# Optimization experiments

Hardware: AMD Instinct MI355X
Metric: run time of the kernel (lower is better)

Reference implementation:

```python
import jax, jax.numpy as jnp
import numpy as np

B, T, C = 512, 128, 384   # batch, seq (== block_size), embed_dim
H, D = 6, 64              # n_heads, head_size
BLOCK_SIZE = 128


def setup_inputs() -> dict:
    key = jax.random.key(0)
    ks = jax.random.split(key, 6)
    s = C ** -0.5  # init scale, values irrelevant to correctness
    x = jax.random.normal(ks[0], (B, T, C), dtype=jnp.float32)
    Wq = jax.random.normal(ks[1], (H, C, D), dtype=jnp.float32) * s
    Wk = jax.random.normal(ks[2], (H, C, D), dtype=jnp.float32) * s
    Wv = jax.random.normal(ks[3], (H, C, D), dtype=jnp.float32) * s
    Wp = jax.random.normal(ks[4], (H * D, C), dtype=jnp.float32) * s
    bp = jax.random.normal(ks[5], (C,), dtype=jnp.float32) * 0.01
    return {"x": x, "Wq": Wq, "Wk": Wk, "Wv": Wv, "Wp": Wp, "bp": bp}


def reference(x, Wq, Wk, Wv, Wp, bp):
    # Forward of MultiHeadAttentionClass (eval mode: dropout disabled).
    # Heads are vectorized instead of the original Python per-head loop.
    Bx, Tx, Cx = x.shape
    x = x[:, :BLOCK_SIZE, :]                       # truncate to block_size
    t = x.shape[1]
    q = jnp.einsum('btc,hcd->bhtd', x, Wq)         # [B,H,T,D]
    k = jnp.einsum('btc,hcd->bhtd', x, Wk)
    v = jnp.einsum('btc,hcd->bhtd', x, Wv)
    scores = jnp.einsum('bhtd,bhsd->bhts', q, k) * (D ** -0.5)  # [B,H,T,T]
    causal = jnp.tril(jnp.ones((t, t), dtype=bool))
    scores = jnp.where(causal[None, None], scores, -jnp.inf)
    wei = jax.nn.softmax(scores, axis=-1)
    out = jnp.einsum('bhts,bhsd->bhtd', wei, v)    # [B,H,T,D]
    out = out.transpose(0, 2, 1, 3).reshape(x.shape[0], t, H * D)  # concat heads
    out = out @ Wp + bp                            # projection to embed_dim
    return out
```

## Files before the change

### kernel.cpp

```cpp
#include <hip/hip_runtime.h>

#define NB 512
#define NTOK 128
#define NC 384
#define NH 6
#define ND 64

typedef short s16x8 __attribute__((ext_vector_type(8)));
typedef float f32x4 __attribute__((ext_vector_type(4)));

#define MFMA16(a, b, c) __builtin_amdgcn_mfma_f32_16x16x32_bf16((a), (b), (c), 0, 0, 0)

static __device__ __forceinline__ unsigned short f2bf(float f) {
  unsigned int u = __builtin_bit_cast(unsigned int, f);
  u = (u + 0x7FFFu + ((u >> 16) & 1u)) >> 16;
  return (unsigned short)u;
}

__global__ __launch_bounds__(256) void convert_weights(
    const float* __restrict__ Wq, const float* __restrict__ Wk,
    const float* __restrict__ Wv, const float* __restrict__ Wp,
    unsigned short* __restrict__ wqkvT, unsigned short* __restrict__ wpT) {
  int idx = blockIdx.x * 256 + threadIdx.x;
  const int NQKV = 3 * NH * ND * NC;
  if (idx < NQKV) {
    int c = idx % NC;
    int d = (idx / NC) % ND;
    int h = (idx / (NC * ND)) % NH;
    int m = idx / (NC * ND * NH);
    const float* W = (m == 0) ? Wq : (m == 1) ? Wk : Wv;
    wqkvT[idx] = f2bf(W[(h * NC + c) * ND + d]);
  } else {
    int j = idx - NQKV;
    int cc = j / NC, r = j % NC;
    wpT[j] = f2bf(Wp[r * NC + cc]);
  }
}

struct SP1 { unsigned short xs[128][40]; unsigned short w[3][64][40]; };
struct SP3 { unsigned short p[128][72]; };

__global__ __launch_bounds__(256, 2) void attn_fused(
    const float* __restrict__ x, const unsigned short* __restrict__ wqkvT,
    unsigned short* __restrict__ O) {
  const int h = blockIdx.x >> 9;
  const int b = blockIdx.x & 511;
  const int tid = threadIdx.x;
  const int lane = tid & 63;
  const int l15 = lane & 15;
  const int lg = lane >> 4;
  const int r0 = (tid >> 6) * 32;

  __shared__ __align__(16) union { SP1 p1; SP3 p3; } su;
  __shared__ __align__(16) unsigned short qs[128][72];
  __shared__ __align__(16) unsigned short ks[128][72];
  __shared__ __align__(16) unsigned short vts[64][144];

  f32x4 accq[2][4], acck[2][4], accv[2][4];
#pragma unroll
  for (int i = 0; i < 2; ++i)
#pragma unroll
    for (int j = 0; j < 4; ++j) {
      accq[i][j] = f32x4{0.f, 0.f, 0.f, 0.f};
      acck[i][j] = f32x4{0.f, 0.f, 0.f, 0.f};
      accv[i][j] = f32x4{0.f, 0.f, 0.f, 0.f};
    }

  const float* xb = x + (size_t)b * (NTOK * NC);
  const unsigned short* wb = wqkvT + h * (ND * NC);

  const int xr = tid >> 3;
  const int xc = (tid & 7) * 4;
  const int wn = tid >> 2;
  const int wc = (tid & 3) * 8;

  for (int kc = 0; kc < 12; ++kc) {
    const int c0 = kc * 32;
    __syncthreads();
#pragma unroll
    for (int s = 0; s < 4; ++s) {
      int row = xr + 32 * s;
      float4 f = *(const float4*)(xb + row * NC + c0 + xc);
      union { unsigned short h4[4]; uint2 u; } t;
      t.h4[0] = f2bf(f.x); t.h4[1] = f2bf(f.y); t.h4[2] = f2bf(f.z); t.h4[3] = f2bf(f.w);
      *(uint2*)&su.p1.xs[row][xc] = t.u;
    }
#pragma unroll
    for (int m = 0; m < 3; ++m) {
      s16x8 w8 = *(const s16x8*)(wb + m * (NH * ND * NC) + wn * NC + c0 + wc);
      *(s16x8*)&su.p1.w[m][wn][wc] = w8;
    }
    __syncthreads();
    s16x8 a0 = *(const s16x8*)&su.p1.xs[r0 + l15][lg * 8];
    s16x8 a1 = *(const s16x8*)&su.p1.xs[r0 + 16 + l15][lg * 8];
#pragma unroll
    for (int nt = 0; nt < 4; ++nt) {
      s16x8 bq = *(const s16x8*)&su.p1.w[0][nt * 16 + l15][lg * 8];
      accq[0][nt] = MFMA16(a0, bq, accq[0][nt]);
      accq[1][nt] = MFMA16(a1, bq, accq[1][nt]);
      s16x8 bk = *(const s16x8*)&su.p1.w[1][nt * 16 + l15][lg * 8];
      acck[0][nt] = MFMA16(a0, bk, acck[0][nt]);
      acck[1][nt] = MFMA16(a1, bk, acck[1][nt]);
      s16x8 bv = *(const s16x8*)&su.p1.w[2][nt * 16 + l15][lg * 8];
      accv[0][nt] = MFMA16(a0, bv, accv[0][nt]);
      accv[1][nt] = MFMA16(a1, bv, accv[1][nt]);
    }
  }

#pragma unroll
  for (int mt = 0; mt < 2; ++mt)
#pragma unroll
    for (int nt = 0; nt < 4; ++nt) {
      int trow = r0 + 16 * mt + 4 * lg;
      int col = 16 * nt + l15;
#pragma unroll
      for (int r = 0; r < 4; ++r) {
        qs[trow + r][col] = f2bf(accq[mt][nt][r] * 0.125f);
        ks[trow + r][col] = f2bf(acck[mt][nt][r]);
      }
      union { unsigned short h4[4]; uint2 u; } t;
#pragma unroll
      for (int r = 0; r < 4; ++r) t.h4[r] = f2bf(accv[mt][nt][r]);
      *(uint2*)&vts[col][trow] = t.u;
    }
  __syncthreads();

  f32x4 sacc[2][8];
#pragma unroll
  for (int i = 0; i < 2; ++i)
#pragma unroll
    for (int j = 0; j < 8; ++j) sacc[i][j] = f32x4{0.f, 0.f, 0.f, 0.f};

#pragma unroll
  for (int kd = 0; kd < 2; ++kd) {
    s16x8 aq0 = *(const s16x8*)&qs[r0 + l15][kd * 32 + lg * 8];
    s16x8 aq1 = *(const s16x8*)&qs[r0 + 16 + l15][kd * 32 + lg * 8];
#pragma unroll
    for (int nt = 0; nt < 8; ++nt) {
      s16x8 bk = *(const s16x8*)&ks[nt * 16 + l15][kd * 32 + lg * 8];
      sacc[0][nt] = MFMA16(aq0, bk, sacc[0][nt]);
      sacc[1][nt] = MFMA16(aq1, bk, sacc[1][nt]);
    }
  }

  float inv_[2][4];
#pragma unroll
  for (int mt = 0; mt < 2; ++mt)
#pragma unroll
    for (int r = 0; r < 4; ++r) {
      int trow = r0 + 16 * mt + 4 * lg + r;
      float mx = -1e30f;
#pragma unroll
      for (int nt = 0; nt < 8; ++nt) {
        bool valid = (nt * 16 + l15) <= trow;
        float v = valid ? sacc[mt][nt][r] : -1e30f;
        sacc[mt][nt][r] = v;
        mx = fmaxf(mx, v);
      }
#pragma unroll
      for (int off = 1; off < 16; off <<= 1) mx = fmaxf(mx, __shfl_xor(mx, off, 64));
      float sm = 0.f;
#pragma unroll
      for (int nt = 0; nt < 8; ++nt) {
        float e = __expf(sacc[mt][nt][r] - mx);
        sacc[mt][nt][r] = e;
        sm += e;
      }
#pragma unroll
      for (int off = 1; off < 16; off <<= 1) sm += __shfl_xor(sm, off, 64);
      inv_[mt][r] = 1.f / sm;
    }

  f32x4 oacc[2][4];
#pragma unroll
  for (int i = 0; i < 2; ++i)
#pragma unroll
    for (int j = 0; j < 4; ++j) oacc[i][j] = f32x4{0.f, 0.f, 0.f, 0.f};

#pragma unroll
  for (int c2 = 0; c2 < 2; ++c2) {
#pragma unroll
    for (int mt = 0; mt < 2; ++mt)
#pragma unroll
      for (int ntl = 0; ntl < 4; ++ntl) {
        int nt = c2 * 4 + ntl;
        int trow = r0 + 16 * mt + 4 * lg;
        int col = ntl * 16 + l15;
#pragma unroll
        for (int r = 0; r < 4; ++r)
          su.p3.p[trow + r][col] = f2bf(sacc[mt][nt][r] * inv_[mt][r]);
      }
    __syncthreads();
#pragma unroll
    for (int ks2 = 0; ks2 < 2; ++ks2) {
      s16x8 ap0 = *(const s16x8*)&su.p3.p[r0 + l15][ks2 * 32 + lg * 8];
      s16x8 ap1 = *(const s16x8*)&su.p3.p[r0 + 16 + l15][ks2 * 32 + lg * 8];
#pragma unroll
      for (int nt = 0; nt < 4; ++nt) {
        s16x8 bv = *(const s16x8*)&vts[nt * 16 + l15][c2 * 64 + ks2 * 32 + lg * 8];
        oacc[0][nt] = MFMA16(ap0, bv, oacc[0][nt]);
        oacc[1][nt] = MFMA16(ap1, bv, oacc[1][nt]);
      }
    }
    __syncthreads();
  }

  unsigned short* Ob = O + ((size_t)b * NTOK) * (NH * ND) + h * ND;
#pragma unroll
  for (int mt = 0; mt < 2; ++mt)
#pragma unroll
    for (int nt = 0; nt < 4; ++nt) {
      int trow = r0 + 16 * mt + 4 * lg;
      int col = nt * 16 + l15;
#pragma unroll
      for (int r = 0; r < 4; ++r)
        Ob[(size_t)(trow + r) * (NH * ND) + col] = f2bf(oacc[mt][nt][r]);
    }
}

__global__ __launch_bounds__(256) void proj_gemm(
    const unsigned short* __restrict__ O, const unsigned short* __restrict__ wpT,
    const float* __restrict__ bp, float* __restrict__ out) {
  const int ntile = blockIdx.x >> 9;
  const int mtile = blockIdx.x & 511;
  const int m0 = mtile * 128, n0 = ntile * 128;
  const int tid = threadIdx.x;
  const int lane = tid & 63;
  const int l15 = lane & 15, lg = lane >> 4;
  const int r0 = (tid >> 6) * 32;

  __shared__ __align__(16) unsigned short as_[128][40];
  __shared__ __align__(16) unsigned short bs_[128][40];

  f32x4 acc[2][8];
#pragma unroll
  for (int i = 0; i < 2; ++i)
#pragma unroll
    for (int j = 0; j < 8; ++j) acc[i][j] = f32x4{0.f, 0.f, 0.f, 0.f};

  const int sr = tid >> 2, sc = (tid & 3) * 8;
  for (int kc = 0; kc < 12; ++kc) {
    int c0 = kc * 32;
    __syncthreads();
#pragma unroll
    for (int s = 0; s < 2; ++s) {
      int row = sr + 64 * s;
      *(s16x8*)&as_[row][sc] = *(const s16x8*)(O + (size_t)(m0 + row) * NC + c0 + sc);
      *(s16x8*)&bs_[row][sc] = *(const s16x8*)(wpT + (size_t)(n0 + row) * NC + c0 + sc);
    }
    __syncthreads();
    s16x8 a0 = *(const s16x8*)&as_[r0 + l15][lg * 8];
    s16x8 a1 = *(const s16x8*)&as_[r0 + 16 + l15][lg * 8];
#pragma unroll
    for (int nt = 0; nt < 8; ++nt) {
      s16x8 bb = *(const s16x8*)&bs_[nt * 16 + l15][lg * 8];
      acc[0][nt] = MFMA16(a0, bb, acc[0][nt]);
      acc[1][nt] = MFMA16(a1, bb, acc[1][nt]);
    }
  }
#pragma unroll
  for (int mt = 0; mt < 2; ++mt)
#pragma unroll
    for (int nt = 0; nt < 8; ++nt) {
      int trow = m0 + r0 + 16 * mt + 4 * lg;
      int col = n0 + nt * 16 + l15;
      float bias = bp[col];
#pragma unroll
      for (int r = 0; r < 4; ++r)
        out[(size_t)(trow + r) * NC + col] = acc[mt][nt][r] + bias;
    }
}

extern "C" void kernel_launch(void* const* d_in, const int* in_sizes, int n_in,
                              void* d_out, int out_size, void* d_ws, size_t ws_size,
                              hipStream_t stream) {
  const float* x  = (const float*)d_in[0];
  const float* Wq = (const float*)d_in[1];
  const float* Wk = (const float*)d_in[2];
  const float* Wv = (const float*)d_in[3];
  const float* Wp = (const float*)d_in[4];
  const float* bp = (const float*)d_in[5];
  float* out = (float*)d_out;

  char* ws = (char*)d_ws;
  unsigned short* O     = (unsigned short*)(ws);
  unsigned short* wqkvT = (unsigned short*)(ws + 50331648);
  unsigned short* wpT   = (unsigned short*)(ws + 51216384);

  convert_weights<<<2304, 256, 0, stream>>>(Wq, Wk, Wv, Wp, wqkvT, wpT);
  attn_fused<<<NB * NH, 256, 0, stream>>>(x, wqkvT, O);
  proj_gemm<<<3 * 512, 256, 0, stream>>>(O, wpT, bp, out);
}
```

Before: 354.5 us.

## Restructure attention kernel: 8 waves, causal tile skipping, register prefetch of global loads

```diff
diff --git a/kernel.cpp b/kernel.cpp
--- a/kernel.cpp
+++ b/kernel.cpp
@@ -15,6 +15,12 @@
   unsigned int u = __builtin_bit_cast(unsigned int, f);
   u = (u + 0x7FFFu + ((u >> 16) & 1u)) >> 16;
   return (unsigned short)u;
+}
+
+static __device__ __forceinline__ uint2 pack4(float a, float b, float c, float d) {
+  union { unsigned short h[4]; uint2 u; } t;
+  t.h[0] = f2bf(a); t.h[1] = f2bf(b); t.h[2] = f2bf(c); t.h[3] = f2bf(d);
+  return t.u;
 }
 
 __global__ __launch_bounds__(256) void convert_weights(
@@ -37,185 +43,181 @@
   }
 }
 
-struct SP1 { unsigned short xs[128][40]; unsigned short w[3][64][40]; };
-struct SP3 { unsigned short p[128][72]; };
-
-__global__ __launch_bounds__(256, 2) void attn_fused(
+__global__ __launch_bounds__(512, 4) void attn_fused(
     const float* __restrict__ x, const unsigned short* __restrict__ wqkvT,
     unsigned short* __restrict__ O) {
-  const int h = blockIdx.x >> 9;
-  const int b = blockIdx.x & 511;
+  const int b = blockIdx.x / NH;
+  const int h = blockIdx.x % NH;
   const int tid = threadIdx.x;
   const int lane = tid & 63;
   const int l15 = lane & 15;
   const int lg = lane >> 4;
-  const int r0 = (tid >> 6) * 32;
-
-  __shared__ __align__(16) union { SP1 p1; SP3 p3; } su;
-  __shared__ __align__(16) unsigned short qs[128][72];
+  const int wid = tid >> 6;
+  const int r0 = wid * 16;
+
+  __shared__ __align__(16) union {
+    struct { unsigned short xs[128][72]; unsigned short w[3][64][72]; } s1;
+    struct { unsigned short qs[128][72]; } s2;
+    struct { unsigned short pB[128][136]; } s3;
+  } u;
   __shared__ __align__(16) unsigned short ks[128][72];
-  __shared__ __align__(16) unsigned short vts[64][144];
-
-  f32x4 accq[2][4], acck[2][4], accv[2][4];
-#pragma unroll
-  for (int i = 0; i < 2; ++i)
-#pragma unroll
-    for (int j = 0; j < 4; ++j) {
-      accq[i][j] = f32x4{0.f, 0.f, 0.f, 0.f};
-      acck[i][j] = f32x4{0.f, 0.f, 0.f, 0.f};
-      accv[i][j] = f32x4{0.f, 0.f, 0.f, 0.f};
-    }
+  __shared__ __align__(16) unsigned short vts[64][136];
+
+  f32x4 accq[4], acck[4], accv[4];
+#pragma unroll
+  for (int j = 0; j < 4; ++j) {
+    accq[j] = f32x4{0.f, 0.f, 0.f, 0.f};
+    acck[j] = f32x4{0.f, 0.f, 0.f, 0.f};
+    accv[j] = f32x4{0.f, 0.f, 0.f, 0.f};
+  }
 
   const float* xb = x + (size_t)b * (NTOK * NC);
-  const unsigned short* wb = wqkvT + h * (ND * NC);
-
-  const int xr = tid >> 3;
-  const int xc = (tid & 7) * 4;
-  const int wn = tid >> 2;
-  const int wc = (tid & 3) * 8;
-
-  for (int kc = 0; kc < 12; ++kc) {
-    const int c0 = kc * 32;
+  const int xrow = tid >> 2;
+  const int xcc = (tid & 3) * 16;
+  const float* xg = xb + xrow * NC + xcc;
+  const int wrow = (tid >> 3) & 63;
+  const int wcc = (tid & 7) * 8;
+  const unsigned short* wg = wqkvT + ((size_t)h * ND + wrow) * NC + wcc;
+  const int WM = NH * ND * NC;
+
+  float4 xa0, xa1, xa2, xa3;
+  s16x8 wa0, wa1, wa2;
+  xa0 = *(const float4*)(xg + 0);  xa1 = *(const float4*)(xg + 4);
+  xa2 = *(const float4*)(xg + 8);  xa3 = *(const float4*)(xg + 12);
+  wa0 = *(const s16x8*)(wg);
+  wa1 = *(const s16x8*)(wg + WM);
+  wa2 = *(const s16x8*)(wg + 2 * WM);
+
+  for (int kc = 0; kc < 6; ++kc) {
     __syncthreads();
-#pragma unroll
-    for (int s = 0; s < 4; ++s) {
-      int row = xr + 32 * s;
-      float4 f = *(const float4*)(xb + row * NC + c0 + xc);
-      union { unsigned short h4[4]; uint2 u; } t;
-      t.h4[0] = f2bf(f.x); t.h4[1] = f2bf(f.y); t.h4[2] = f2bf(f.z); t.h4[3] = f2bf(f.w);
-      *(uint2*)&su.p1.xs[row][xc] = t.u;
-    }
-#pragma unroll
-    for (int m = 0; m < 3; ++m) {
-      s16x8 w8 = *(const s16x8*)(wb + m * (NH * ND * NC) + wn * NC + c0 + wc);
-      *(s16x8*)&su.p1.w[m][wn][wc] = w8;
-    }
+    union { unsigned short hh[8]; s16x8 v; } t0, t1;
+    t0.hh[0] = f2bf(xa0.x); t0.hh[1] = f2bf(xa0.y); t0.hh[2] = f2bf(xa0.z); t0.hh[3] = f2bf(xa0.w);
+    t0.hh[4] = f2bf(xa1.x); t0.hh[5] = f2bf(xa1.y); t0.hh[6] = f2bf(xa1.z); t0.hh[7] = f2bf(xa1.w);
+    t1.hh[0] = f2bf(xa2.x); t1.hh[1] = f2bf(xa2.y); t1.hh[2] = f2bf(xa2.z); t1.hh[3] = f2bf(xa2.w);
+    t1.hh[4] = f2bf(xa3.x); t1.hh[5] = f2bf(xa3.y); t1.hh[6] = f2bf(xa3.z); t1.hh[7] = f2bf(xa3.w);
+    *(s16x8*)&u.s1.xs[xrow][xcc] = t0.v;
+    *(s16x8*)&u.s1.xs[xrow][xcc + 8] = t1.v;
+    *(s16x8*)&u.s1.w[0][wrow][wcc] = wa0;
+    *(s16x8*)&u.s1.w[1][wrow][wcc] = wa1;
+    *(s16x8*)&u.s1.w[2][wrow][wcc] = wa2;
     __syncthreads();
-    s16x8 a0 = *(const s16x8*)&su.p1.xs[r0 + l15][lg * 8];
-    s16x8 a1 = *(const s16x8*)&su.p1.xs[r0 + 16 + l15][lg * 8];
-#pragma unroll
-    for (int nt = 0; nt < 4; ++nt) {
-      s16x8 bq = *(const s16x8*)&su.p1.w[0][nt * 16 + l15][lg * 8];
-      accq[0][nt] = MFMA16(a0, bq, accq[0][nt]);
-      accq[1][nt] = MFMA16(a1, bq, accq[1][nt]);
-      s16x8 bk = *(const s16x8*)&su.p1.w[1][nt * 16 + l15][lg * 8];
-      acck[0][nt] = MFMA16(a0, bk, acck[0][nt]);
-      acck[1][nt] = MFMA16(a1, bk, acck[1][nt]);
-      s16x8 bv = *(const s16x8*)&su.p1.w[2][nt * 16 + l15][lg * 8];
-      accv[0][nt] = MFMA16(a0, bv, accv[0][nt]);
-      accv[1][nt] = MFMA16(a1, bv, accv[1][nt]);
-    }
-  }
-
-#pragma unroll
-  for (int mt = 0; mt < 2; ++mt)
-#pragma unroll
-    for (int nt = 0; nt < 4; ++nt) {
-      int trow = r0 + 16 * mt + 4 * lg;
-      int col = 16 * nt + l15;
+    if (kc < 5) {
+      xg += 64; wg += 64;
+      xa0 = *(const float4*)(xg + 0);  xa1 = *(const float4*)(xg + 4);
+      xa2 = *(const float4*)(xg + 8);  xa3 = *(const float4*)(xg + 12);
+      wa0 = *(const s16x8*)(wg);
+      wa1 = *(const s16x8*)(wg + WM);
+      wa2 = *(const s16x8*)(wg + 2 * WM);
+    }
+#pragma unroll
+    for (int kd = 0; kd < 2; ++kd) {
+      s16x8 a = *(const s16x8*)&u.s1.xs[r0 + l15][kd * 32 + lg * 8];
+#pragma unroll
+      for (int nt = 0; nt < 4; ++nt) {
+        s16x8 bq = *(const s16x8*)&u.s1.w[0][nt * 16 + l15][kd * 32 + lg * 8];
+        accq[nt] = MFMA16(a, bq, accq[nt]);
+        s16x8 bk = *(const s16x8*)&u.s1.w[1][nt * 16 + l15][kd * 32 + lg * 8];
+        acck[nt] = MFMA16(a, bk, acck[nt]);
+        s16x8 bv = *(const s16x8*)&u.s1.w[2][nt * 16 + l15][kd * 32 + lg * 8];
+        accv[nt] = MFMA16(a, bv, accv[nt]);
+      }
+    }
+  }
+
+  __syncthreads();
+#pragma unroll
+  for (int nt = 0; nt < 4; ++nt) {
+    int col = nt * 16 + l15;
+#pragma unroll
+    for (int r = 0; r < 4; ++r) {
+      int row = r0 + 4 * lg + r;
+      u.s2.qs[row][col] = f2bf(accq[nt][r] * 0.125f);
+      ks[row][col] = f2bf(acck[nt][r]);
+    }
+    *(uint2*)&vts[col][r0 + 4 * lg] =
+        pack4(accv[nt][0], accv[nt][1], accv[nt][2], accv[nt][3]);
+  }
+  __syncthreads();
+
+  f32x4 sacc[8];
+#pragma unroll
+  for (int j = 0; j < 8; ++j) sacc[j] = f32x4{0.f, 0.f, 0.f, 0.f};
+
+#pragma unroll
+  for (int kd = 0; kd < 2; ++kd) {
+    s16x8 bq = *(const s16x8*)&u.s2.qs[r0 + l15][kd * 32 + lg * 8];
+#pragma unroll
+    for (int nt = 0; nt < 8; ++nt) {
+      if (nt <= wid) {
+        s16x8 ak = *(const s16x8*)&ks[nt * 16 + l15][kd * 32 + lg * 8];
+        sacc[nt] = MFMA16(ak, bq, sacc[nt]);
+      }
+    }
+  }
+
+  const int q = r0 + l15;
+  float mx = -1e30f;
+#pragma unroll
+  for (int nt = 0; nt < 8; ++nt) {
+    if (nt <= wid) {
 #pragma unroll
       for (int r = 0; r < 4; ++r) {
-        qs[trow + r][col] = f2bf(accq[mt][nt][r] * 0.125f);
-        ks[trow + r][col] = f2bf(acck[mt][nt][r]);
-      }
-      union { unsigned short h4[4]; uint2 u; } t;
-#pragma unroll
-      for (int r = 0; r < 4; ++r) t.h4[r] = f2bf(accv[mt][nt][r]);
-      *(uint2*)&vts[col][trow] = t.u;
-    }
+        int s = nt * 16 + 4 * lg + r;
+        float v = (s <= q) ? sacc[nt][r] : -1e30f;
+        sacc[nt][r] = v;
+        mx = fmaxf(mx, v);
+      }
+    }
+  }
+  mx = fmaxf(mx, __shfl_xor(mx, 16, 64));
+  mx = fmaxf(mx, __shfl_xor(mx, 32, 64));
+  float sm = 0.f;
+#pragma unroll
+  for (int nt = 0; nt < 8; ++nt) {
+    if (nt <= wid) {
+#pragma unroll
+      for (int r = 0; r < 4; ++r) {
+        float e = __expf(sacc[nt][r] - mx);
+        sacc[nt][r] = e;
+        sm += e;
+      }
+    }
+  }
+  sm += __shfl_xor(sm, 16, 64);
+  sm += __shfl_xor(sm, 32, 64);
+  float inv = 1.f / sm;
+
   __syncthreads();
-
-  f32x4 sacc[2][8];
-#pragma unroll
-  for (int i = 0; i < 2; ++i)
-#pragma unroll
-    for (int j = 0; j < 8; ++j) sacc[i][j] = f32x4{0.f, 0.f, 0.f, 0.f};
-
-#pragma unroll
-  for (int kd = 0; kd < 2; ++kd) {
-    s16x8 aq0 = *(const s16x8*)&qs[r0 + l15][kd * 32 + lg * 8];
-    s16x8 aq1 = *(const s16x8*)&qs[r0 + 16 + l15][kd * 32 + lg * 8];
-#pragma unroll
-    for (int nt = 0; nt < 8; ++nt) {
-      s16x8 bk = *(const s16x8*)&ks[nt * 16 + l15][kd * 32 + lg * 8];
-      sacc[0][nt] = MFMA16(aq0, bk, sacc[0][nt]);
-      sacc[1][nt] = MFMA16(aq1, bk, sacc[1][nt]);
-    }
-  }
-
-  float inv_[2][4];
-#pragma unroll
-  for (int mt = 0; mt < 2; ++mt)
-#pragma unroll
-    for (int r = 0; r < 4; ++r) {
-      int trow = r0 + 16 * mt + 4 * lg + r;
-      float mx = -1e30f;
-#pragma unroll
-      for (int nt = 0; nt < 8; ++nt) {
-        bool valid = (nt * 16 + l15) <= trow;
-        float v = valid ? sacc[mt][nt][r] : -1e30f;
-        sacc[mt][nt][r] = v;
-        mx = fmaxf(mx, v);
-      }
-#pragma unroll
-      for (int off = 1; off < 16; off <<= 1) mx = fmaxf(mx, __shfl_xor(mx, off, 64));
-      float sm = 0.f;
-#pragma unroll
-      for (int nt = 0; nt < 8; ++nt) {
-        float e = __expf(sacc[mt][nt][r] - mx);
-        sacc[mt][nt][r] = e;
-        sm += e;
-      }
-#pragma unroll
-      for (int off = 1; off < 16; off <<= 1) sm += __shfl_xor(sm, off, 64);
-      inv_[mt][r] = 1.f / sm;
-    }
-
-  f32x4 oacc[2][4];
-#pragma unroll
-  for (int i = 0; i < 2; ++i)
-#pragma unroll
-    for (int j = 0; j < 4; ++j) oacc[i][j] = f32x4{0.f, 0.f, 0.f, 0.f};
-
-#pragma unroll
-  for (int c2 = 0; c2 < 2; ++c2) {
-#pragma unroll
-    for (int mt = 0; mt < 2; ++mt)
-#pragma unroll
-      for (int ntl = 0; ntl < 4; ++ntl) {
-        int nt = c2 * 4 + ntl;
-        int trow = r0 + 16 * mt + 4 * lg;
-        int col = ntl * 16 + l15;
-#pragma unroll
-        for (int r = 0; r < 4; ++r)
-          su.p3.p[trow + r][col] = f2bf(sacc[mt][nt][r] * inv_[mt][r]);
-      }
-    __syncthreads();
-#pragma unroll
-    for (int ks2 = 0; ks2 < 2; ++ks2) {
-      s16x8 ap0 = *(const s16x8*)&su.p3.p[r0 + l15][ks2 * 32 + lg * 8];
-      s16x8 ap1 = *(const s16x8*)&su.p3.p[r0 + 16 + l15][ks2 * 32 + lg * 8];
-#pragma unroll
-      for (int nt = 0; nt < 4; ++nt) {
-        s16x8 bv = *(const s16x8*)&vts[nt * 16 + l15][c2 * 64 + ks2 * 32 + lg * 8];
-        oacc[0][nt] = MFMA16(ap0, bv, oacc[0][nt]);
-        oacc[1][nt] = MFMA16(ap1, bv, oacc[1][nt]);
-      }
-    }
-    __syncthreads();
-  }
-
-  unsigned short* Ob = O + ((size_t)b * NTOK) * (NH * ND) + h * ND;
-#pragma unroll
-  for (int mt = 0; mt < 2; ++mt)
-#pragma unroll
-    for (int nt = 0; nt < 4; ++nt) {
-      int trow = r0 + 16 * mt + 4 * lg;
-      int col = nt * 16 + l15;
-#pragma unroll
-      for (int r = 0; r < 4; ++r)
-        Ob[(size_t)(trow + r) * (NH * ND) + col] = f2bf(oacc[mt][nt][r]);
-    }
+#pragma unroll
+  for (int nt = 0; nt < 8; ++nt) {
+    uint2 pv;
+    if (nt <= wid)
+      pv = pack4(sacc[nt][0] * inv, sacc[nt][1] * inv, sacc[nt][2] * inv, sacc[nt][3] * inv);
+    else { pv.x = 0u; pv.y = 0u; }
+    *(uint2*)&u.s3.pB[r0 + l15][nt * 16 + 4 * lg] = pv;
+  }
+  __syncthreads();
+
+  f32x4 oacc[4];
+#pragma unroll
+  for (int j = 0; j < 4; ++j) oacc[j] = f32x4{0.f, 0.f, 0.f, 0.f};
+#pragma unroll
+  for (int kd = 0; kd < 4; ++kd) {
+    if (kd * 32 <= r0 + 15) {
+      s16x8 bp = *(const s16x8*)&u.s3.pB[r0 + l15][kd * 32 + lg * 8];
+#pragma unroll
+      for (int dt = 0; dt < 4; ++dt) {
+        s16x8 av = *(const s16x8*)&vts[dt * 16 + l15][kd * 32 + lg * 8];
+        oacc[dt] = MFMA16(av, bp, oacc[dt]);
+      }
+    }
+  }
+
+  unsigned short* Op = O + ((size_t)(b * NTOK) + r0 + l15) * (NH * ND) + h * ND;
+#pragma unroll
+  for (int dt = 0; dt < 4; ++dt)
+    *(uint2*)&Op[dt * 16 + 4 * lg] =
+        pack4(oacc[dt][0], oacc[dt][1], oacc[dt][2], oacc[dt][3]);
 }
 
 __global__ __launch_bounds__(256) void proj_gemm(
@@ -239,16 +241,23 @@
     for (int j = 0; j < 8; ++j) acc[i][j] = f32x4{0.f, 0.f, 0.f, 0.f};
 
   const int sr = tid >> 2, sc = (tid & 3) * 8;
+  const unsigned short* ag = O + (size_t)(m0 + sr) * NC + sc;
+  const unsigned short* bg = wpT + (size_t)(n0 + sr) * NC + sc;
+  s16x8 ar0 = *(const s16x8*)ag;
+  s16x8 ar1 = *(const s16x8*)(ag + (size_t)64 * NC);
+  s16x8 br0 = *(const s16x8*)bg;
+  s16x8 br1 = *(const s16x8*)(bg + (size_t)64 * NC);
+
   for (int kc = 0; kc < 12; ++kc) {
-    int c0 = kc * 32;
     __syncthreads();
-#pragma unroll
-    for (int s = 0; s < 2; ++s) {
-      int row = sr + 64 * s;
-      *(s16x8*)&as_[row][sc] = *(const s16x8*)(O + (size_t)(m0 + row) * NC + c0 + sc);
-      *(s16x8*)&bs_[row][sc] = *(const s16x8*)(wpT + (size_t)(n0 + row) * NC + c0 + sc);
-    }
+    *(s16x8*)&as_[sr][sc] = ar0;  *(s16x8*)&as_[sr + 64][sc] = ar1;
+    *(s16x8*)&bs_[sr][sc] = br0;  *(s16x8*)&bs_[sr + 64][sc] = br1;
     __syncthreads();
+    if (kc < 11) {
+      ag += 32; bg += 32;
+      ar0 = *(const s16x8*)ag;  ar1 = *(const s16x8*)(ag + (size_t)64 * NC);
+      br0 = *(const s16x8*)bg;  br1 = *(const s16x8*)(bg + (size_t)64 * NC);
+    }
     s16x8 a0 = *(const s16x8*)&as_[r0 + l15][lg * 8];
     s16x8 a1 = *(const s16x8*)&as_[r0 + 16 + l15][lg * 8];
 #pragma unroll
@@ -288,6 +297,6 @@
   unsigned short* wpT   = (unsigned short*)(ws + 51216384);
 
   convert_weights<<<2304, 256, 0, stream>>>(Wq, Wk, Wv, Wp, wqkvT, wpT);
-  attn_fused<<<NB * NH, 256, 0, stream>>>(x, wqkvT, O);
+  attn_fused<<<NB * NH, 512, 0, stream>>>(x, wqkvT, O);
   proj_gemm<<<3 * 512, 256, 0, stream>>>(O, wpT, bp, out);
 }
```

New measurement: 864.2 us. 144% more time.
